# Optimization experiments

Hardware: AMD Instinct MI355X
Metric: run time of the kernel (lower is better)

Reference implementation:

```python
import jax, jax.numpy as jnp
import numpy as np

STRIDE = 1
MAX_STRIDE = 250  # 25 * 10 default


def setup_inputs() -> dict:
    key = jax.random.key(0)
    k1, k2 = jax.random.split(key)
    T = 1_000_000
    prediction = jax.random.normal(k1, (T,), dtype=jnp.float32)
    ground_truth = jax.random.normal(k2, (T,), dtype=jnp.float32)
    return {"prediction": prediction, "ground_truth": ground_truth}


def reference(prediction, ground_truth):
    T = prediction.shape[0]
    lags = jnp.arange(0, MAX_STRIDE, STRIDE)
    idx = jnp.arange(T)

    # ground-truth statistics are lag-independent
    mean_gt = jnp.mean(ground_truth)
    var_gt = jnp.var(ground_truth, ddof=1)  # torch.var is unbiased
    v_gt = ground_truth - mean_gt

    def ccc_at_lag(n):
        # shifted pred: n leading zeros followed by prediction[:-n]
        src = idx - n
        pred = jnp.where(src >= 0, prediction[jnp.clip(src, 0)], 0.0)
        mean_pred = jnp.mean(pred)
        var_pred = jnp.var(pred, ddof=1)
        cov = jnp.mean((pred - mean_pred) * v_gt)  # population covariance
        denom = var_gt + var_pred + (mean_gt - mean_pred) ** 2
        return 2.0 * cov / denom

    cccs = jax.vmap(ccc_at_lag)(lags)  # [n_lags]
    return 1.0 - jnp.mean(cccs)
```

## Files before the change

kernel.cpp:

```cpp
#include <hip/hip_runtime.h>
#include <hip/hip_bf16.h>


#define TC 4096
#define NTHR 512
#define NLAG 256
#define NUSED 250
#define NREP 16
#define GT4 (TC / 4 + 66)
#define STATREP_OFF (NREP * NLAG)
#define COUNTER_OFF (STATREP_OFF + NREP * 16)

typedef float f2 __attribute__((ext_vector_type(2)));

__device__ __forceinline__ float4 ld_gt_sw(const float* s_gt, int i4) {
    int s = i4 ^ ((i4 >> 3) & 7);
    return *(const float4*)&s_gt[4 * s];
}

__device__ __forceinline__ float ld_atomic(const float* p) {
    return __hip_atomic_load(p, __ATOMIC_RELAXED, __HIP_MEMORY_SCOPE_AGENT);
}

__global__ __launch_bounds__(NTHR) void ccc_fused(const float* __restrict__ pred,
                                                  const float* __restrict__ gt,
                                                  float* __restrict__ ws,
                                                  float* __restrict__ out,
                                                  int T, int nch) {
    __shared__ __align__(16) float s_pred[TC];
    __shared__ __align__(16) float s_gt[GT4 * 4];
    __shared__ __align__(16) float s_acc[16][NLAG];
    __shared__ float s_red[8][4];
    __shared__ float s_stats[4];
    __shared__ float s_sp64[64];
    __shared__ unsigned s_last;

    const int tid = threadIdx.x;
    const int c = blockIdx.x;
    const int j0 = c * TC;

    float sp = 0.f, qp = 0.f, sg = 0.f, qg = 0.f;
    if (j0 + 4 * GT4 <= T) {
        #pragma unroll 2
        for (int i4 = tid; i4 < TC / 4; i4 += NTHR) {
            float4 v = *(const float4*)&pred[j0 + 4 * i4];
            *(float4*)&s_pred[4 * i4] = v;
            sp += v.x + v.y + v.z + v.w;
            qp += v.x * v.x + v.y * v.y + v.z * v.z + v.w * v.w;
        }
        #pragma unroll 2
        for (int i4 = tid; i4 < GT4; i4 += NTHR) {
            float4 v = *(const float4*)&gt[j0 + 4 * i4];
            int s = i4 ^ ((i4 >> 3) & 7);
            *(float4*)&s_gt[4 * s] = v;
            if (i4 < TC / 4) {
                sg += v.x + v.y + v.z + v.w;
                qg += v.x * v.x + v.y * v.y + v.z * v.z + v.w * v.w;
            }
        }
    } else {
        #pragma unroll 2
        for (int i4 = tid; i4 < TC / 4; i4 += NTHR) {
            int g = j0 + 4 * i4;
            float4 v = make_float4(0.f, 0.f, 0.f, 0.f);
            if (g + 3 < T) v = *(const float4*)&pred[g];
            *(float4*)&s_pred[4 * i4] = v;
            sp += v.x + v.y + v.z + v.w;
            qp += v.x * v.x + v.y * v.y + v.z * v.z + v.w * v.w;
        }
        #pragma unroll 2
        for (int i4 = tid; i4 < GT4; i4 += NTHR) {
            int g = j0 + 4 * i4;
            float4 v = make_float4(0.f, 0.f, 0.f, 0.f);
            if (g + 3 < T) v = *(const float4*)&gt[g];
            int s = i4 ^ ((i4 >> 3) & 7);
            *(float4*)&s_gt[4 * s] = v;
            if (i4 < TC / 4) {
                sg += v.x + v.y + v.z + v.w;
                qg += v.x * v.x + v.y * v.y + v.z * v.z + v.w * v.w;
            }
        }
    }
    __syncthreads();

    const int sub = tid >> 5;
    const int l = tid & 31;
    int gi = sub * 64 + 2 * l;
    const int pi0 = sub * 64;

    f2 E[6], O[5];
    {
        float4 a = ld_gt_sw(s_gt, gi);
        float4 b = ld_gt_sw(s_gt, gi + 1);
        float4 d = ld_gt_sw(s_gt, gi + 2);
        E[0] = f2{a.x, a.y}; E[1] = f2{a.z, a.w};
        E[2] = f2{b.x, b.y}; E[3] = f2{b.z, b.w};
        E[4] = f2{d.x, d.y}; E[5] = f2{d.z, d.w};
        O[0] = f2{a.y, a.z}; O[1] = f2{a.w, b.x};
        O[2] = f2{b.y, b.z}; O[3] = f2{b.w, d.x};
        O[4] = f2{d.y, d.z};
    }
    f2 acc2[8];
    #pragma unroll
    for (int k = 0; k < 8; ++k) acc2[k] = f2{0.f, 0.f};

    #pragma unroll 8
    for (int it = 0; it < 64; ++it) {
        float4 nw = ld_gt_sw(s_gt, gi + 3 + it);
        float4 p = *(const float4*)&s_pred[4 * (pi0 + it)];
        f2 pA = f2{p.x, p.y}, pB = f2{p.z, p.w};
        #pragma unroll
        for (int m = 0; m < 4; ++m) {
            acc2[2 * m]     = __builtin_elementwise_fma(pA, E[m],     acc2[2 * m]);
            acc2[2 * m]     = __builtin_elementwise_fma(pB, E[m + 1], acc2[2 * m]);
            acc2[2 * m + 1] = __builtin_elementwise_fma(pA, O[m],     acc2[2 * m + 1]);
            acc2[2 * m + 1] = __builtin_elementwise_fma(pB, O[m + 1], acc2[2 * m + 1]);
        }
        float w11 = E[5].y;
        E[0] = E[2]; E[1] = E[3]; E[2] = E[4]; E[3] = E[5];
        E[4] = f2{nw.x, nw.y}; E[5] = f2{nw.z, nw.w};
        O[0] = O[2]; O[1] = O[3]; O[2] = O[4];
        O[3] = f2{w11, nw.x}; O[4] = f2{nw.y, nw.z};
    }

    const int wv = tid >> 6, ln = tid & 63;
    #pragma unroll
    for (int off = 32; off > 0; off >>= 1) {
        sp += __shfl_down(sp, off, 64);
        qp += __shfl_down(qp, off, 64);
        sg += __shfl_down(sg, off, 64);
        qg += __shfl_down(qg, off, 64);
    }
    if (ln == 0) { s_red[wv][0] = sp; s_red[wv][1] = qp; s_red[wv][2] = sg; s_red[wv][3] = qg; }

    #pragma unroll
    for (int k = 0; k < 8; ++k) s_acc[sub][8 * l + k] = acc2[k].x + acc2[k].y;
    __syncthreads();

    const int rep = c & (NREP - 1);
    if (tid < NLAG) {
        float lagsum = 0.f;
        #pragma unroll
        for (int s = 0; s < 16; ++s) lagsum += s_acc[s][tid];
        atomicAdd(&ws[rep * NLAG + tid], lagsum);
    }
    if (tid < 4) {
        float v = 0.f;
        #pragma unroll
        for (int w8 = 0; w8 < 8; ++w8) v += s_red[w8][tid];
        atomicAdd(&ws[STATREP_OFF + rep * 16 + tid], v);
    }

    __syncthreads();
    if (tid == 0) {
        unsigned* cnt = (unsigned*)(ws + COUNTER_OFF);
        unsigned old = __hip_atomic_fetch_add(cnt, 1u, __ATOMIC_RELAXED,
                                              __HIP_MEMORY_SCOPE_AGENT);
        unsigned want_poison = 0xAAAAAAAAu + (unsigned)(nch - 1);
        unsigned want_zero = (unsigned)(nch - 1);
        s_last = (old == want_poison || old == want_zero) ? 1u : 0u;
    }
    __syncthreads();
    if (!s_last) return;

    {
        const int lag = tid & 255, h = tid >> 8;
        float a = 0.f;
        #pragma unroll
        for (int r = 8 * h; r < 8 * h + 8; ++r) a += ld_atomic(&ws[r * NLAG + lag]);
        s_acc[h][lag] = a;
    }
    if (tid < 64) s_sp64[tid] = ld_atomic(&ws[STATREP_OFF + (tid >> 2) * 16 + (tid & 3)]);
    if (tid < NLAG) {
        float x = pred[T - NLAG + tid];
        s_pred[tid] = x;
        s_acc[2][tid] = x;
        s_acc[4][tid] = x * x;
    }
    __syncthreads();

    if (tid < 4) {
        float s = 0.f;
        #pragma unroll
        for (int r = 0; r < 16; ++r) s += s_sp64[4 * r + tid];
        s_stats[tid] = s;
    }

    float *sa = s_acc[2], *sb = s_acc[3], *qa = s_acc[4], *qb = s_acc[5];
    for (int d = 1; d < NLAG; d <<= 1) {
        __syncthreads();
        if (tid < NLAG) {
            sb[tid] = sa[tid] + ((tid + d < NLAG) ? sa[tid + d] : 0.f);
            qb[tid] = qa[tid] + ((tid + d < NLAG) ? qa[tid + d] : 0.f);
        }
        float* tmp = sa; sa = sb; sb = tmp;
        tmp = qa; qa = qb; qb = tmp;
    }
    __syncthreads();

    if (tid < NLAG) {
        float lagC = s_acc[0][tid] + s_acc[1][tid];
        float v = 0.f;
        if (tid < NUSED) {
            const float Tf = (float)T;
            float sum_pred = s_stats[0], sumsq_pred = s_stats[1];
            float sum_gt = s_stats[2], sumsq_gt = s_stats[3];
            float mean_gt = sum_gt / Tf;
            float var_gt = (sumsq_gt - sum_gt * sum_gt / Tf) / (Tf - 1.f);
            float tail_s = (tid == 0) ? 0.f : sa[NLAG - tid];
            float tail_q = (tid == 0) ? 0.f : qa[NLAG - tid];
            float S = sum_pred - tail_s;
            float Q = sumsq_pred - tail_q;
            float mean_p = S / Tf;
            float var_p = (Q - S * S / Tf) / (Tf - 1.f);
            float cov = (lagC - mean_gt * S) / Tf;
            float dm = mean_gt - mean_p;
            v = 2.f * cov / (var_gt + var_p + dm * dm);
        }
        s_acc[6][tid] = v;
    }
    __syncthreads();
    for (int s = 128; s > 0; s >>= 1) {
        if (tid < s) s_acc[6][tid] += s_acc[6][tid + s];
        __syncthreads();
    }
    if (tid == 0) out[0] = 1.f - s_acc[6][0] / (float)NUSED;
}

extern "C" void kernel_launch(void* const* d_in, const int* in_sizes, int n_in,
                              void* d_out, int out_size, void* d_ws, size_t ws_size,
                              hipStream_t stream) {
    const float* pred = (const float*)d_in[0];
    const float* gt   = (const float*)d_in[1];
    float* out = (float*)d_out;
    float* ws  = (float*)d_ws;
    const int T = in_sizes[0];
    const int nch = (T + TC - 1) / TC;

    ccc_fused<<<nch, NTHR, 0, stream>>>(pred, gt, ws, out, T, nch);
}
```

Baseline: 71.85 us.

## Widen per-thread lag register tile and replace tail scans with wave shuffles

Each thread now accumulates 16 lags over 32 shared-memory steps instead of 8 lags over 64. That halves the LDS loads per packed FMA and reuses each loaded prediction vector across twice as many lags. The prediction tile gets per-subgroup padding, and the accumulator writes to shared memory are XOR-swizzled to cut bank conflicts. The final-block suffix sums and the closing reduction use wave shuffles instead of repeated __syncthreads shared-memory scans. In exchange, register pressure rises and the cross-subgroup reduction now sums 32 partial rows instead of 16.

```diff
diff --git a/kernel.cpp b/kernel.cpp
--- a/kernel.cpp
+++ b/kernel.cpp
@@ -10,12 +10,23 @@
 #define GT4 (TC / 4 + 66)
 #define STATREP_OFF (NREP * NLAG)
 #define COUNTER_OFF (STATREP_OFF + NREP * 16)
+#define NSUB 32
+#define PPAD 132
 
 typedef float f2 __attribute__((ext_vector_type(2)));
 
 __device__ __forceinline__ float4 ld_gt_sw(const float* s_gt, int i4) {
     int s = i4 ^ ((i4 >> 3) & 7);
     return *(const float4*)&s_gt[4 * s];
+}
+
+__device__ __forceinline__ void st_gt_sw(float* s_gt, int i4, float4 v) {
+    int s = i4 ^ ((i4 >> 3) & 7);
+    *(float4*)&s_gt[4 * s] = v;
+}
+
+__device__ __forceinline__ int pred_off(int i4) {
+    return 4 * i4 + 4 * (i4 >> 5);
 }
 
 __device__ __forceinline__ float ld_atomic(const float* p) {
@@ -27,9 +38,9 @@
                                                   float* __restrict__ ws,
                                                   float* __restrict__ out,
                                                   int T, int nch) {
-    __shared__ __align__(16) float s_pred[TC];
+    __shared__ __align__(16) float s_pred[NSUB * PPAD];
     __shared__ __align__(16) float s_gt[GT4 * 4];
-    __shared__ __align__(16) float s_acc[16][NLAG];
+    __shared__ __align__(16) float s_acc[NSUB][NLAG];
     __shared__ float s_red[8][4];
     __shared__ float s_stats[4];
     __shared__ float s_sp64[64];
@@ -44,15 +55,14 @@
         #pragma unroll 2
         for (int i4 = tid; i4 < TC / 4; i4 += NTHR) {
             float4 v = *(const float4*)&pred[j0 + 4 * i4];
-            *(float4*)&s_pred[4 * i4] = v;
+            *(float4*)&s_pred[pred_off(i4)] = v;
             sp += v.x + v.y + v.z + v.w;
             qp += v.x * v.x + v.y * v.y + v.z * v.z + v.w * v.w;
         }
         #pragma unroll 2
         for (int i4 = tid; i4 < GT4; i4 += NTHR) {
             float4 v = *(const float4*)&gt[j0 + 4 * i4];
-            int s = i4 ^ ((i4 >> 3) & 7);
-            *(float4*)&s_gt[4 * s] = v;
+            st_gt_sw(s_gt, i4, v);
             if (i4 < TC / 4) {
                 sg += v.x + v.y + v.z + v.w;
                 qg += v.x * v.x + v.y * v.y + v.z * v.z + v.w * v.w;
@@ -64,7 +74,7 @@
             int g = j0 + 4 * i4;
             float4 v = make_float4(0.f, 0.f, 0.f, 0.f);
             if (g + 3 < T) v = *(const float4*)&pred[g];
-            *(float4*)&s_pred[4 * i4] = v;
+            *(float4*)&s_pred[pred_off(i4)] = v;
             sp += v.x + v.y + v.z + v.w;
             qp += v.x * v.x + v.y * v.y + v.z * v.z + v.w * v.w;
         }
@@ -73,8 +83,7 @@
             int g = j0 + 4 * i4;
             float4 v = make_float4(0.f, 0.f, 0.f, 0.f);
             if (g + 3 < T) v = *(const float4*)&gt[g];
-            int s = i4 ^ ((i4 >> 3) & 7);
-            *(float4*)&s_gt[4 * s] = v;
+            st_gt_sw(s_gt, i4, v);
             if (i4 < TC / 4) {
                 sg += v.x + v.y + v.z + v.w;
                 qg += v.x * v.x + v.y * v.y + v.z * v.z + v.w * v.w;
@@ -83,44 +92,52 @@
     }
     __syncthreads();
 
-    const int sub = tid >> 5;
-    const int l = tid & 31;
-    int gi = sub * 64 + 2 * l;
-    const int pi0 = sub * 64;
-
-    f2 E[6], O[5];
+    const int sub = tid >> 4;
+    const int l = tid & 15;
+    int gi = sub * 32 + 4 * l;
+    const float* pbase = &s_pred[sub * PPAD];
+
+    f2 E[10], O[9];
     {
         float4 a = ld_gt_sw(s_gt, gi);
         float4 b = ld_gt_sw(s_gt, gi + 1);
         float4 d = ld_gt_sw(s_gt, gi + 2);
+        float4 e = ld_gt_sw(s_gt, gi + 3);
+        float4 f = ld_gt_sw(s_gt, gi + 4);
         E[0] = f2{a.x, a.y}; E[1] = f2{a.z, a.w};
         E[2] = f2{b.x, b.y}; E[3] = f2{b.z, b.w};
         E[4] = f2{d.x, d.y}; E[5] = f2{d.z, d.w};
+        E[6] = f2{e.x, e.y}; E[7] = f2{e.z, e.w};
+        E[8] = f2{f.x, f.y}; E[9] = f2{f.z, f.w};
         O[0] = f2{a.y, a.z}; O[1] = f2{a.w, b.x};
         O[2] = f2{b.y, b.z}; O[3] = f2{b.w, d.x};
-        O[4] = f2{d.y, d.z};
-    }
-    f2 acc2[8];
-    #pragma unroll
-    for (int k = 0; k < 8; ++k) acc2[k] = f2{0.f, 0.f};
+        O[4] = f2{d.y, d.z}; O[5] = f2{d.w, e.x};
+        O[6] = f2{e.y, e.z}; O[7] = f2{e.w, f.x};
+        O[8] = f2{f.y, f.z};
+    }
+    f2 acc2[16];
+    #pragma unroll
+    for (int k = 0; k < 16; ++k) acc2[k] = f2{0.f, 0.f};
 
     #pragma unroll 8
-    for (int it = 0; it < 64; ++it) {
-        float4 nw = ld_gt_sw(s_gt, gi + 3 + it);
-        float4 p = *(const float4*)&s_pred[4 * (pi0 + it)];
+    for (int it = 0; it < 32; ++it) {
+        float4 nw = ld_gt_sw(s_gt, gi + 5 + it);
+        float4 p = *(const float4*)&pbase[4 * it];
         f2 pA = f2{p.x, p.y}, pB = f2{p.z, p.w};
         #pragma unroll
-        for (int m = 0; m < 4; ++m) {
+        for (int m = 0; m < 8; ++m) {
             acc2[2 * m]     = __builtin_elementwise_fma(pA, E[m],     acc2[2 * m]);
             acc2[2 * m]     = __builtin_elementwise_fma(pB, E[m + 1], acc2[2 * m]);
             acc2[2 * m + 1] = __builtin_elementwise_fma(pA, O[m],     acc2[2 * m + 1]);
             acc2[2 * m + 1] = __builtin_elementwise_fma(pB, O[m + 1], acc2[2 * m + 1]);
         }
-        float w11 = E[5].y;
-        E[0] = E[2]; E[1] = E[3]; E[2] = E[4]; E[3] = E[5];
-        E[4] = f2{nw.x, nw.y}; E[5] = f2{nw.z, nw.w};
-        O[0] = O[2]; O[1] = O[3]; O[2] = O[4];
-        O[3] = f2{w11, nw.x}; O[4] = f2{nw.y, nw.z};
+        float w19 = E[9].y;
+        #pragma unroll
+        for (int q2 = 0; q2 < 8; ++q2) E[q2] = E[q2 + 2];
+        E[8] = f2{nw.x, nw.y}; E[9] = f2{nw.z, nw.w};
+        #pragma unroll
+        for (int q2 = 0; q2 < 7; ++q2) O[q2] = O[q2 + 2];
+        O[7] = f2{w19, nw.x}; O[8] = f2{nw.y, nw.z};
     }
 
     const int wv = tid >> 6, ln = tid & 63;
@@ -134,15 +151,17 @@
     if (ln == 0) { s_red[wv][0] = sp; s_red[wv][1] = qp; s_red[wv][2] = sg; s_red[wv][3] = qg; }
 
     #pragma unroll
-    for (int k = 0; k < 8; ++k) s_acc[sub][8 * l + k] = acc2[k].x + acc2[k].y;
+    for (int k = 0; k < 16; ++k)
+        s_acc[sub][(l << 4) | (k ^ l)] = acc2[k].x + acc2[k].y;
     __syncthreads();
 
     const int rep = c & (NREP - 1);
     if (tid < NLAG) {
         float lagsum = 0.f;
         #pragma unroll
-        for (int s = 0; s < 16; ++s) lagsum += s_acc[s][tid];
-        atomicAdd(&ws[rep * NLAG + tid], lagsum);
+        for (int s2 = 0; s2 < NSUB; ++s2) lagsum += s_acc[s2][tid];
+        int lag = (tid & 0xF0) | ((tid ^ (tid >> 4)) & 15);
+        atomicAdd(&ws[rep * NLAG + lag], lagsum);
     }
     if (tid < 4) {
         float v = 0.f;
@@ -171,60 +190,64 @@
         s_acc[h][lag] = a;
     }
     if (tid < 64) s_sp64[tid] = ld_atomic(&ws[STATREP_OFF + (tid >> 2) * 16 + (tid & 3)]);
+
+    float tx = 0.f, tq = 0.f;
     if (tid < NLAG) {
-        float x = pred[T - NLAG + tid];
-        s_pred[tid] = x;
-        s_acc[2][tid] = x;
-        s_acc[4][tid] = x * x;
-    }
+        float t = pred[T - NLAG + tid];
+        tx = t; tq = t * t;
+    }
+    #pragma unroll
+    for (int d = 1; d < 64; d <<= 1) {
+        float xs = __shfl_down(tx, d, 64);
+        float qs = __shfl_down(tq, d, 64);
+        if (ln + d < 64) { tx += xs; tq += qs; }
+    }
+    if (ln == 0) { s_red[wv][0] = tx; s_red[wv][1] = tq; }
     __syncthreads();
 
     if (tid < 4) {
-        float s = 0.f;
-        #pragma unroll
-        for (int r = 0; r < 16; ++r) s += s_sp64[4 * r + tid];
-        s_stats[tid] = s;
-    }
-
-    float *sa = s_acc[2], *sb = s_acc[3], *qa = s_acc[4], *qb = s_acc[5];
-    for (int d = 1; d < NLAG; d <<= 1) {
-        __syncthreads();
-        if (tid < NLAG) {
-            sb[tid] = sa[tid] + ((tid + d < NLAG) ? sa[tid + d] : 0.f);
-            qb[tid] = qa[tid] + ((tid + d < NLAG) ? qa[tid + d] : 0.f);
-        }
-        float* tmp = sa; sa = sb; sb = tmp;
-        tmp = qa; qa = qb; qb = tmp;
-    }
-    __syncthreads();
-
+        float s2 = 0.f;
+        #pragma unroll
+        for (int r = 0; r < 16; ++r) s2 += s_sp64[4 * r + tid];
+        s_stats[tid] = s2;
+    }
     if (tid < NLAG) {
+        #pragma unroll
+        for (int w2 = 1; w2 < 4; ++w2)
+            if (w2 > wv) { tx += s_red[w2][0]; tq += s_red[w2][1]; }
+        s_acc[2][tid] = tx;
+        s_acc[3][tid] = tq;
+    }
+    __syncthreads();
+
+    float v = 0.f;
+    if (tid < NUSED) {
+        const float Tf = (float)T;
+        float sum_pred = s_stats[0], sumsq_pred = s_stats[1];
+        float sum_gt = s_stats[2], sumsq_gt = s_stats[3];
+        float mean_gt = sum_gt / Tf;
+        float var_gt = (sumsq_gt - sum_gt * sum_gt / Tf) / (Tf - 1.f);
         float lagC = s_acc[0][tid] + s_acc[1][tid];
-        float v = 0.f;
-        if (tid < NUSED) {
-            const float Tf = (float)T;
-            float sum_pred = s_stats[0], sumsq_pred = s_stats[1];
-            float sum_gt = s_stats[2], sumsq_gt = s_stats[3];
-            float mean_gt = sum_gt / Tf;
-            float var_gt = (sumsq_gt - sum_gt * sum_gt / Tf) / (Tf - 1.f);
-            float tail_s = (tid == 0) ? 0.f : sa[NLAG - tid];
-            float tail_q = (tid == 0) ? 0.f : qa[NLAG - tid];
-            float S = sum_pred - tail_s;
-            float Q = sumsq_pred - tail_q;
-            float mean_p = S / Tf;
-            float var_p = (Q - S * S / Tf) / (Tf - 1.f);
-            float cov = (lagC - mean_gt * S) / Tf;
-            float dm = mean_gt - mean_p;
-            v = 2.f * cov / (var_gt + var_p + dm * dm);
-        }
-        s_acc[6][tid] = v;
-    }
-    __syncthreads();
-    for (int s = 128; s > 0; s >>= 1) {
-        if (tid < s) s_acc[6][tid] += s_acc[6][tid + s];
-        __syncthreads();
-    }
-    if (tid == 0) out[0] = 1.f - s_acc[6][0] / (float)NUSED;
+        float tail_s = (tid == 0) ? 0.f : s_acc[2][NLAG - tid];
+        float tail_q = (tid == 0) ? 0.f : s_acc[3][NLAG - tid];
+        float S = sum_pred - tail_s;
+        float Q = sumsq_pred - tail_q;
+        float mean_p = S / Tf;
+        float var_p = (Q - S * S / Tf) / (Tf - 1.f);
+        float cov = (lagC - mean_gt * S) / Tf;
+        float dm = mean_gt - mean_p;
+        v = 2.f * cov / (var_gt + var_p + dm * dm);
+    }
+    #pragma unroll
+    for (int off = 32; off > 0; off >>= 1) v += __shfl_down(v, off, 64);
+    if (ln == 0) s_red[wv][2] = v;
+    __syncthreads();
+    if (tid == 0) {
+        float s2 = 0.f;
+        #pragma unroll
+        for (int w2 = 0; w2 < 8; ++w2) s2 += s_red[w2][2];
+        out[0] = 1.f - s2 / (float)NUSED;
+    }
 }
 
 extern "C" void kernel_launch(void* const* d_in, const int* in_sizes, int n_in,
```

Result: faster. 70.00 us (-2.6%).
